# Performance work log

Measured on AMD Instinct MI355X. Metric: run time of the kernel, lower is better.

The kernel has to match this reference:

```python
import jax, jax.numpy as jnp
import numpy as np

B, NB, BIN = 8, 512, 10           # batch, num_bins, bin_size
D, H, L, F, E, K = 1024, 8, 4, 1024, 30, 4  # emb, heads, layers, ffn, experts, top_k
S = NB + 1                        # seq len with CLS token
DH = D // H
CAP = 1152


def _pos_encoding(seq, d):
    pos = np.arange(seq)[:, None].astype(np.float32)
    div = np.exp(np.arange(0, d, 2).astype(np.float32) * (-np.log(10000.0) / d))
    pe = np.zeros((seq, d), dtype=np.float32)
    pe[:, 0::2] = np.sin(pos * div)
    pe[:, 1::2] = np.cos(pos * div)
    return jnp.asarray(pe)

PE = _pos_encoding(S, D)


def _ln(h, g, b):
    m = h.mean(-1, keepdims=True)
    v = ((h - m) ** 2).mean(-1, keepdims=True)
    return (h - m) * jax.lax.rsqrt(v + 1e-5) * g + b


def _conv(h, w, dil):
    # torch Conv1d(k=3, padding=dil, dilation=dil, bias=False) -> same length
    return jax.lax.conv_general_dilated(h, w, (1,), [(dil, dil)], rhs_dilation=(dil,),
                                        dimension_numbers=('NCH', 'OIH', 'NCH'))


def _moe(m, Wg, Bg, W1, B1, W2, B2):
    # top-k routed expert FFN with capacity-based dispatch (no dense all-expert compute)
    T = B * S
    xt = m.reshape(T, D)
    probs = jax.nn.softmax(xt @ Wg + Bg, axis=-1)           # [T, E]
    gate, idx = jax.lax.top_k(probs, K)                     # [T, K]
    gate = gate / gate.sum(-1, keepdims=True)
    e = idx.reshape(-1)                                     # [T*K]
    g = gate.reshape(-1)
    oh = jax.nn.one_hot(e, E, dtype=jnp.int32)
    pos = (jnp.cumsum(oh, axis=0) * oh).sum(-1) - 1         # position within expert
    keep = pos < CAP
    pos_c = jnp.where(keep, pos, CAP)                       # overflow -> dummy slot CAP
    xt_rep = xt[jnp.repeat(jnp.arange(T), K)]               # [T*K, D]
    buf = jnp.zeros((E, CAP + 1, D), m.dtype).at[e, pos_c].add(xt_rep)
    hid = jax.nn.gelu(jnp.einsum('ecd,edf->ecf', buf, W1) + B1[:, None, :], approximate=False)
    out = jnp.einsum('ecf,efd->ecd', hid, W2) + B2[:, None, :]
    y = out[e, pos_c] * (g * keep)[:, None]                 # dropped tokens masked to 0
    return y.reshape(T, K, D).sum(1).reshape(B, S, D)


def _layer(h, p):
    (l1g, l1b, l2g, l2b, Wq, Wk, Wv, Wo, Bq, Bk, Bv, Bo, Wg, Bg, We1, Be1, We2, Be2) = p
    a = _ln(h, l1g, l1b)
    q = (a @ Wq + Bq).reshape(B, S, H, DH)
    k = (a @ Wk + Bk).reshape(B, S, H, DH)
    v = (a @ Wv + Bv).reshape(B, S, H, DH)
    att = jax.nn.softmax(jnp.einsum('bqhd,bkhd->bhqk', q, k) / np.sqrt(DH), axis=-1)
    o = jnp.einsum('bhqk,bkhd->bqhd', att, v).reshape(B, S, D) @ Wo + Bo
    h = h + o
    m = _ln(h, l2g, l2b)
    h = h + _moe(m, Wg, Bg, We1, Be1, We2, Be2)
    return h, None


def _fwd(x, conv_w1, conv_w2, conv_w3, bn1_g, bn1_b, bn2_g, bn2_b, bn3_g, bn3_b,
         proj_w, proj_b, cls_token, mask_token, ln1_g, ln1_b, ln2_g, ln2_b,
         wq, wk, wv, wo, bq, bk, bv, bo, wg, bg, we1, be1, we2, be2):
    x3 = x.reshape(B, NB, BIN)
    h = x3.reshape(B * NB, 1, BIN)
    bn_scale = np.float32(1.0 / np.sqrt(1.0 + 1e-5))  # eval BN: running mean 0, var 1
    for w, gm, bt, dil in ((conv_w1, bn1_g, bn1_b, 1), (conv_w2, bn2_g, bn2_b, 2), (conv_w3, bn3_g, bn3_b, 4)):
        h = _conv(h, w, dil)
        h = h * (gm * bn_scale)[None, :, None] + bt[None, :, None]
        h = jax.nn.gelu(h, approximate=False)
    h = h.mean(-1)                                   # AdaptiveAvgPool1d(1)
    emb = (h @ proj_w + proj_b).reshape(B, NB, D)
    msk = jnp.all(x3 == -100.0, axis=-1)[..., None]
    emb = jnp.where(msk, mask_token, emb)
    emb = jnp.concatenate([jnp.broadcast_to(cls_token, (B, 1, D)), emb], axis=1)
    emb = emb + PE[None]
    h, _ = jax.lax.scan(_layer, emb, (ln1_g, ln1_b, ln2_g, ln2_b, wq, wk, wv, wo,
                                      bq, bk, bv, bo, wg, bg, we1, be1, we2, be2))
    return h[:, 0, :]


def setup_inputs() -> dict:
    key = jax.random.key(0)
    ks = iter(jax.random.split(key, 40))
    r = lambda shape, s=0.02: jax.random.normal(next(ks), shape, jnp.float32) * s
    return dict(
        x=jax.random.normal(next(ks), (B, NB * BIN), jnp.float32),
        conv_w1=r((16, 1, 3), 0.3), conv_w2=r((32, 16, 3), 0.15), conv_w3=r((64, 32, 3), 0.1),
        bn1_g=jnp.ones((16,)), bn1_b=jnp.zeros((16,)),
        bn2_g=jnp.ones((32,)), bn2_b=jnp.zeros((32,)),
        bn3_g=jnp.ones((64,)), bn3_b=jnp.zeros((64,)),
        proj_w=r((64, D), 0.05), proj_b=jnp.zeros((D,)),
        cls_token=r((1, 1, D)), mask_token=r((1, 1, D)),
        ln1_g=jnp.ones((L, D)), ln1_b=jnp.zeros((L, D)),
        ln2_g=jnp.ones((L, D)), ln2_b=jnp.zeros((L, D)),
        wq=r((L, D, D)), wk=r((L, D, D)), wv=r((L, D, D)), wo=r((L, D, D)),
        bq=jnp.zeros((L, D)), bk=jnp.zeros((L, D)), bv=jnp.zeros((L, D)), bo=jnp.zeros((L, D)),
        wg=r((L, D, E)), bg=jnp.zeros((L, E)),
        we1=r((L, E, D, F)), be1=jnp.zeros((L, E, F)),
        we2=r((L, E, F, D)), be2=jnp.zeros((L, E, D)),
    )


def reference(x, conv_w1, conv_w2, conv_w3, bn1_g, bn1_b, bn2_g, bn2_b, bn3_g, bn3_b,
              proj_w, proj_b, cls_token, mask_token, ln1_g, ln1_b, ln2_g, ln2_b,
              wq, wk, wv, wo, bq, bk, bv, bo, wg, bg, we1, be1, we2, be2):
    return _fwd(x, conv_w1, conv_w2, conv_w3, bn1_g, bn1_b, bn2_g, bn2_b, bn3_g, bn3_b,
                proj_w, proj_b, cls_token, mask_token, ln1_g, ln1_b, ln2_g, ln2_b,
                wq, wk, wv, wo, bq, bk, bv, bo, wg, bg, we1, be1, we2, be2)
```

## Files before the change

### kernel.cpp

```cpp
#include <hip/hip_runtime.h>
#include <hip/hip_bf16.h>
#include <math.h>

#define BATCH   8
#define NBINS   512
#define BINSZ   10
#define DMODEL  1024
#define NHEAD   8
#define DHEAD   128
#define NLAYER  4
#define NEXP    30
#define TOPK    4
#define SEQ     513
#define NTOK    (BATCH*SEQ)
#define NBINTOT (BATCH*NBINS)
#define CAPACITY 1152
#define TKF     (NTOK*TOPK)

typedef __attribute__((ext_vector_type(8))) __bf16 bf16x8;
typedef __attribute__((ext_vector_type(4))) __bf16 bf16x4;
typedef __attribute__((ext_vector_type(4))) float f32x4;

__device__ __forceinline__ float gelu_f(float x) {
  return 0.5f * x * (1.0f + erff(x * 0.7071067811865475f));
}

__device__ __forceinline__ bf16x8 bf8_zero() {
  int4 z = make_int4(0, 0, 0, 0);
  return __builtin_bit_cast(bf16x8, z);
}

__global__ __launch_bounds__(256) void transpose_w(const float* __restrict__ src,
                                                   __bf16* __restrict__ dst) {
  int mat = blockIdx.y;
  int tile = blockIdx.x;
  int kt = (tile >> 4) * 64;
  int nt = (tile & 15) * 64;
  const float* s = src + (size_t)mat * 1024 * 1024;
  __bf16* d = dst + (size_t)mat * 1024 * 1024;
  __shared__ float t[64][65];
  int tid = threadIdx.x;
  int r = tid >> 4, c4 = (tid & 15) * 4;
#pragma unroll
  for (int i = 0; i < 4; i++) {
    float4 v = *(const float4*)(s + (size_t)(kt + r + i*16) * 1024 + nt + c4);
    t[r + i*16][c4+0] = v.x; t[r + i*16][c4+1] = v.y;
    t[r + i*16][c4+2] = v.z; t[r + i*16][c4+3] = v.w;
  }
  __syncthreads();
  int r2 = tid >> 2, c2 = (tid & 3) * 16;
  bf16x8 o0, o1;
#pragma unroll
  for (int j = 0; j < 8; j++) { o0[j] = (__bf16)t[c2+j][r2]; o1[j] = (__bf16)t[c2+8+j][r2]; }
  *(bf16x8*)(d + (size_t)(nt + r2) * 1024 + kt + c2)     = o0;
  *(bf16x8*)(d + (size_t)(nt + r2) * 1024 + kt + c2 + 8) = o1;
}

#define CSTEP(acc, T, DIL, hr, wA, wB, wC) { \
  float vv_ = (wB) * (hr)[T]; \
  if ((T) >= (DIL)) vv_ = fmaf((wA), (hr)[(T)-(DIL)], vv_); \
  if ((T) + (DIL) <= 9) vv_ = fmaf((wC), (hr)[(T)+(DIL)], vv_); \
  acc += vv_; }

#define CALL10(DIL, hr, wA, wB, wC) \
  CSTEP(t0,0,DIL,hr,wA,wB,wC); CSTEP(t1,1,DIL,hr,wA,wB,wC); \
  CSTEP(t2,2,DIL,hr,wA,wB,wC); CSTEP(t3,3,DIL,hr,wA,wB,wC); \
  CSTEP(t4,4,DIL,hr,wA,wB,wC); CSTEP(t5,5,DIL,hr,wA,wB,wC); \
  CSTEP(t6,6,DIL,hr,wA,wB,wC); CSTEP(t7,7,DIL,hr,wA,wB,wC); \
  CSTEP(t8,8,DIL,hr,wA,wB,wC); CSTEP(t9,9,DIL,hr,wA,wB,wC);

#define ZERO10 float t0=0.f,t1=0.f,t2=0.f,t3=0.f,t4=0.f,t5=0.f,t6=0.f,t7=0.f,t8=0.f,t9=0.f;

#define STORE10(dst, sc, sh) \
  (dst)[0]=gelu_f(t0*(sc)+(sh)); (dst)[1]=gelu_f(t1*(sc)+(sh)); \
  (dst)[2]=gelu_f(t2*(sc)+(sh)); (dst)[3]=gelu_f(t3*(sc)+(sh)); \
  (dst)[4]=gelu_f(t4*(sc)+(sh)); (dst)[5]=gelu_f(t5*(sc)+(sh)); \
  (dst)[6]=gelu_f(t6*(sc)+(sh)); (dst)[7]=gelu_f(t7*(sc)+(sh)); \
  (dst)[8]=gelu_f(t8*(sc)+(sh)); (dst)[9]=gelu_f(t9*(sc)+(sh));

__global__ __launch_bounds__(64) void conv_frontend(const float* __restrict__ x,
                              const float* __restrict__ w1, const float* __restrict__ w2,
                              const float* __restrict__ w3,
                              const float* __restrict__ g1, const float* __restrict__ b1,
                              const float* __restrict__ g2, const float* __restrict__ b2,
                              const float* __restrict__ g3, const float* __restrict__ b3,
                              float* __restrict__ feat, int* __restrict__ msk) {
  const float bnscale = 0.9999950000374997f;
  int bin = blockIdx.x;
  int c = threadIdx.x;
  __shared__ float xs[BINSZ];
  __shared__ float h1[16][BINSZ];
  __shared__ float h2[32][BINSZ];
  if (c < BINSZ) xs[c] = x[bin*BINSZ + c];
  if (c == 0) {
    int all = 1;
    for (int t = 0; t < BINSZ; t++) if (x[bin*BINSZ+t] != -100.0f) { all = 0; break; }
    msk[bin] = all;
  }
  __syncthreads();
  if (c < 16) {
    float sc = g1[c]*bnscale, sh = b1[c];
    float wA = w1[c*3], wB = w1[c*3+1], wC = w1[c*3+2];
    const float* hr = &xs[0];
    ZERO10;
    CALL10(1, hr, wA, wB, wC);
    STORE10(&h1[c][0], sc, sh);
  }
  __syncthreads();
  if (c < 32) {
    float sc = g2[c]*bnscale, sh = b2[c];
    ZERO10;
    for (int ci = 0; ci < 16; ci++) {
      const float* w = w2 + (c*16+ci)*3;
      float wA = w[0], wB = w[1], wC = w[2];
      const float* hr = &h1[ci][0];
      CALL10(2, hr, wA, wB, wC);
    }
    STORE10(&h2[c][0], sc, sh);
  }
  __syncthreads();
  {
    float sc = g3[c]*bnscale, sh = b3[c];
    ZERO10;
    for (int ci = 0; ci < 32; ci++) {
      const float* w = w3 + (c*32+ci)*3;
      float wA = w[0], wB = w[1], wC = w[2];
      const float* hr = &h2[ci][0];
      CALL10(4, hr, wA, wB, wC);
    }
    float mean = gelu_f(t0*sc+sh) + gelu_f(t1*sc+sh) + gelu_f(t2*sc+sh)
               + gelu_f(t3*sc+sh) + gelu_f(t4*sc+sh) + gelu_f(t5*sc+sh)
               + gelu_f(t6*sc+sh) + gelu_f(t7*sc+sh) + gelu_f(t8*sc+sh)
               + gelu_f(t9*sc+sh);
    feat[bin*64 + c] = mean * 0.1f;
  }
}

__global__ void embed_kernel(const float* __restrict__ feat, const int* __restrict__ msk,
                             const float* __restrict__ proj_w, const float* __restrict__ proj_b,
                             const float* __restrict__ cls_token, const float* __restrict__ mask_token,
                             float* __restrict__ h) {
  int s_ = blockIdx.x;
  int b  = blockIdx.y;
  int tid = threadIdx.x;
  __shared__ __align__(16) float fs[64];
  float out[4];
  if (s_ == 0) {
#pragma unroll
    for (int u = 0; u < 4; u++) out[u] = cls_token[tid*4+u];
  } else {
    int bin = b*NBINS + (s_-1);
    if (tid < 16) ((float4*)fs)[tid] = ((const float4*)(feat + (size_t)bin*64))[tid];
    __syncthreads();
    int m_ = msk[bin];
#pragma unroll
    for (int u = 0; u < 4; u++) {
      int d = tid*4+u;
      float acc = proj_b[d];
      for (int ci = 0; ci < 64; ci++) acc = fmaf(fs[ci], proj_w[ci*DMODEL + d], acc);
      out[u] = m_ ? mask_token[d] : acc;
    }
  }
  const float c0 = -0.008994473019507992f;
#pragma unroll
  for (int u = 0; u < 4; u++) {
    int d = tid*4+u;
    float div = expf(c0 * (float)(d & ~1));
    float ang = (float)s_ * div;
    float pe = (d & 1) ? cosf(ang) : sinf(ang);
    h[((size_t)(b*SEQ + s_))*DMODEL + d] = out[u] + pe;
  }
}

__global__ void ln_kernel(const float* __restrict__ x, float* __restrict__ out,
                          __bf16* __restrict__ outb,
                          const float* __restrict__ g, const float* __restrict__ b) {
  int t = blockIdx.x, tid = threadIdx.x;
  float4 v = ((const float4*)(x + (size_t)t*DMODEL))[tid];
  float s  = v.x+v.y+v.z+v.w;
  float sq = v.x*v.x+v.y*v.y+v.z*v.z+v.w*v.w;
  for (int off = 32; off; off >>= 1) { s += __shfl_down(s, off); sq += __shfl_down(sq, off); }
  __shared__ float ss[4], ssq[4], mv[2];
  int w = tid >> 6, l = tid & 63;
  if (l == 0) { ss[w] = s; ssq[w] = sq; }
  __syncthreads();
  if (tid == 0) {
    float a = 0, c = 0;
    for (int i = 0; i < 4; i++) { a += ss[i]; c += ssq[i]; }
    float mean = a * (1.f/DMODEL);
    float var  = c * (1.f/DMODEL) - mean*mean;
    mv[0] = mean; mv[1] = rsqrtf(var + 1e-5f);
  }
  __syncthreads();
  float mean = mv[0], inv = mv[1];
  float4 gg = ((const float4*)g)[tid];
  float4 bb = ((const float4*)b)[tid];
  float4 o;
  o.x = (v.x-mean)*inv*gg.x + bb.x;
  o.y = (v.y-mean)*inv*gg.y + bb.y;
  o.z = (v.z-mean)*inv*gg.z + bb.z;
  o.w = (v.w-mean)*inv*gg.w + bb.w;
  ((float4*)(out + (size_t)t*DMODEL))[tid] = o;
  bf16x4 ob;
  ob[0] = (__bf16)o.x; ob[1] = (__bf16)o.y; ob[2] = (__bf16)o.z; ob[3] = (__bf16)o.w;
  *(bf16x4*)(outb + (size_t)t*DMODEL + tid*4) = ob;
}

template<int MODE>
__global__ __launch_bounds__(512) void gemm_bf16(
    const __bf16* __restrict__ A, const __bf16* __restrict__ Wt,
    const float* __restrict__ bias, void* __restrict__ C, int M,
    const int* __restrict__ rowmap, const int* __restrict__ cnt,
    const float* __restrict__ gate) {
  int tid = threadIdx.x;
  int rowbase, validrows, e = 0;
  const __bf16* Wb = Wt;
  if (MODE <= 1) {
    rowbase = blockIdx.x * 128;
    validrows = M - rowbase; if (validrows > 128) validrows = 128;
  } else {
    e = blockIdx.x / 9;
    int p0 = (blockIdx.x % 9) * 128;
    int ce = cnt[e];
    if (p0 >= ce) return;
    rowbase = p0;
    validrows = ce - p0; if (validrows > 128) validrows = 128;
    Wb = Wt + (size_t)e * 1024 * 1024;
  }
  int colbase = blockIdx.y * 128;

  __shared__ __align__(16) __bf16 As[4][128][8];
  __shared__ __align__(16) __bf16 Bs[4][128][8];
  __shared__ int srcrow[128];
  __shared__ int frow[128];

  if (tid < 128) {
    if (MODE <= 1) { srcrow[tid] = rowbase + tid; frow[tid] = rowbase + tid; }
    else if (tid < validrows) {
      int f = rowmap[e*CAPACITY + rowbase + tid];
      frow[tid] = f;
      srcrow[tid] = (MODE == 2) ? (f >> 2) : f;
    } else { frow[tid] = 0; srcrow[tid] = 0; }
  }
  __syncthreads();

  int arow = tid >> 2, ag = tid & 3;
  int wcol = tid & 127, wgp = tid >> 7;
  bool aval = (arow < validrows);
  const __bf16* Ap = A + (size_t)srcrow[arow] * 1024 + ag * 8;
  const __bf16* Wp = Wb + (size_t)(colbase + wcol) * 1024 + wgp * 8;

  int w  = tid >> 6;
  int wr = w & 3, wc = w >> 2;
  int l  = tid & 63;
  int lr = l & 15, lg = l >> 4;

  f32x4 acc[2][4] = {};

  bf16x8 areg = bf8_zero(), breg;
  if (aval) areg = *(const bf16x8*)(Ap);
  breg = *(const bf16x8*)(Wp);

  for (int kt = 0; kt < 1024; kt += 32) {
    __syncthreads();
    *(bf16x8*)&As[ag][arow][0] = areg;
    *(bf16x8*)&Bs[wgp][wcol][0] = breg;
    __syncthreads();

    if (kt + 32 < 1024) {
      if (aval) areg = *(const bf16x8*)(Ap + kt + 32);
      breg = *(const bf16x8*)(Wp + kt + 32);
    }

    bf16x8 af[2], bf[4];
    af[0] = *(const bf16x8*)&As[lg][wr*32 + lr][0];
    af[1] = *(const bf16x8*)&As[lg][wr*32 + 16 + lr][0];
#pragma unroll
    for (int fj = 0; fj < 4; fj++) bf[fj] = *(const bf16x8*)&Bs[lg][wc*64 + fj*16 + lr][0];
#pragma unroll
    for (int fi = 0; fi < 2; fi++)
#pragma unroll
      for (int fj = 0; fj < 4; fj++)
        acc[fi][fj] = __builtin_amdgcn_mfma_f32_16x16x32_bf16(af[fi], bf[fj], acc[fi][fj], 0, 0, 0);
  }

  const float* bptr = (MODE >= 2) ? (bias + (size_t)e * 1024) : bias;
#pragma unroll
  for (int fj = 0; fj < 4; fj++) {
    int col = wc*64 + fj*16 + lr;
    float bvv = bptr[colbase + col];
#pragma unroll
    for (int fi = 0; fi < 2; fi++) {
#pragma unroll
      for (int i = 0; i < 4; i++) {
        int r = wr*32 + fi*16 + lg*4 + i;
        if (r >= validrows) continue;
        float val = acc[fi][fj][i] + bvv;
        if (MODE == 0) {
          ((__bf16*)C)[(size_t)(rowbase + r)*1024 + colbase + col] = (__bf16)val;
        } else if (MODE == 1) {
          float* p = (float*)C + (size_t)(rowbase + r)*1024 + colbase + col;
          *p = *p + val;
        } else if (MODE == 2) {
          ((__bf16*)C)[(size_t)frow[r]*1024 + colbase + col] = (__bf16)gelu_f(val);
        } else {
          ((float*)C)[(size_t)frow[r]*1024 + colbase + col] = gate[frow[r]] * val;
        }
      }
    }
  }
}

__global__ __launch_bounds__(256) void attn_mfma(const __bf16* __restrict__ q,
                                                 const __bf16* __restrict__ k,
                                                 const __bf16* __restrict__ v,
                                                 __bf16* __restrict__ o) {
  int qt = blockIdx.x;
  int bh = blockIdx.y;
  int b = bh >> 3, hh = bh & 7;
  int tid = threadIdx.x;
  int wid = tid >> 6, l = tid & 63;
  int lr = l & 15, lg = l >> 4;

  __shared__ __align__(16) __bf16 Ks[64*128];
  __shared__ __align__(16) __bf16 Vt[128*64];

  const float scale = 0.08838834764831845f;

  int qtok = qt*64 + wid*16 + lr;
  int qtokc = qtok < SEQ ? qtok : SEQ-1;
  const __bf16* qrow = q + ((size_t)(b*SEQ + qtokc))*DMODEL + hh*DHEAD;
  bf16x8 qf[4];
#pragma unroll
  for (int c = 0; c < 4; c++) qf[c] = *(const bf16x8*)(qrow + c*32 + lg*8);

  float mreg = -1e30f, lsum = 0.f;
  f32x4 Oacc[8] = {};

  int krow = tid & 63, kdc = tid >> 6;
  int vd = tid & 127, vkg0 = tid >> 7;

  for (int kt = 0; kt < 9; kt++) {
    int kt0 = kt*64;
    __syncthreads();
    {
      int tok = kt0 + krow; if (tok >= SEQ) tok = SEQ-1;
      const __bf16* kr = k + ((size_t)(b*SEQ + tok))*DMODEL + hh*DHEAD + kdc*32;
#pragma unroll
      for (int s2 = 0; s2 < 4; s2++) {
        bf16x8 t = *(const bf16x8*)(kr + s2*8);
        int byte = (krow*256 + (kdc*32 + s2*8)*2) ^ ((krow & 7) << 4);
        *(bf16x8*)((char*)Ks + byte) = t;
      }
    }
    {
#pragma unroll
      for (int it = 0; it < 4; it++) {
        int kkg = vkg0 + it*2;
        bf16x8 t;
#pragma unroll
        for (int j = 0; j < 8; j++) {
          int tok = kt0 + kkg*8 + j; if (tok >= SEQ) tok = SEQ-1;
          t[j] = v[((size_t)(b*SEQ + tok))*DMODEL + hh*DHEAD + vd];
        }
        int byte = (vd*128 + kkg*16) ^ ((vd & 7) << 4);
        *(bf16x8*)((char*)Vt + byte) = t;
      }
    }
    __syncthreads();

    f32x4 sacc[4] = {};
#pragma unroll
    for (int c = 0; c < 4; c++) {
#pragma unroll
      for (int jb = 0; jb < 4; jb++) {
        int row = jb*16 + lr;
        int byte = (row*256 + (c*32 + lg*8)*2) ^ ((lr & 7) << 4);
        bf16x8 af = *(const bf16x8*)((const char*)Ks + byte);
        sacc[jb] = __builtin_amdgcn_mfma_f32_16x16x32_bf16(af, qf[c], sacc[jb], 0, 0, 0);
      }
    }

    float sv[4][4];
    float mt = -1e30f;
#pragma unroll
    for (int jb = 0; jb < 4; jb++)
#pragma unroll
      for (int i = 0; i < 4; i++) {
        int kkI = kt0 + jb*16 + lg*4 + i;
        float s = sacc[jb][i] * scale;
        if (kkI >= SEQ) s = -1e30f;
        sv[jb][i] = s;
        mt = fmaxf(mt, s);
      }
    mt = fmaxf(mt, __shfl_xor(mt, 16));
    mt = fmaxf(mt, __shfl_xor(mt, 32));
    float mnew = fmaxf(mreg, mt);
    float alpha = expf(mreg - mnew);
    float rs = 0.f;
#pragma unroll
    for (int jb = 0; jb < 4; jb++)
#pragma unroll
      for (int i = 0; i < 4; i++) {
        float p = expf(sv[jb][i] - mnew);
        sv[jb][i] = p; rs += p;
      }
    rs += __shfl_xor(rs, 16);
    rs += __shfl_xor(rs, 32);
    lsum = lsum * alpha + rs;
    mreg = mnew;

    unsigned pk[4][2];
#pragma unroll
    for (int jb = 0; jb < 4; jb++) {
      unsigned short c0 = __builtin_bit_cast(unsigned short, (__bf16)sv[jb][0]);
      unsigned short c1 = __builtin_bit_cast(unsigned short, (__bf16)sv[jb][1]);
      unsigned short c2 = __builtin_bit_cast(unsigned short, (__bf16)sv[jb][2]);
      unsigned short c3 = __builtin_bit_cast(unsigned short, (__bf16)sv[jb][3]);
      pk[jb][0] = ((unsigned)c1 << 16) | c0;
      pk[jb][1] = ((unsigned)c3 << 16) | c2;
    }

    float al0 = __shfl(alpha, lg*4 + 0);
    float al1 = __shfl(alpha, lg*4 + 1);
    float al2 = __shfl(alpha, lg*4 + 2);
    float al3 = __shfl(alpha, lg*4 + 3);
#pragma unroll
    for (int db = 0; db < 8; db++) {
      Oacc[db][0] *= al0; Oacc[db][1] *= al1; Oacc[db][2] *= al2; Oacc[db][3] *= al3;
    }

    int srcA = lr + ((lg & 1) << 5);
    int srcB = srcA + 16;
    bool hiSel = (lg >> 1) != 0;
#pragma unroll
    for (int c = 0; c < 2; c++) {
      int a00 = __shfl((int)pk[2*c][0], srcA);
      int a01 = __shfl((int)pk[2*c][1], srcA);
      int a10 = __shfl((int)pk[2*c+1][0], srcA);
      int a11 = __shfl((int)pk[2*c+1][1], srcA);
      int b00 = __shfl((int)pk[2*c][0], srcB);
      int b01 = __shfl((int)pk[2*c][1], srcB);
      int b10 = __shfl((int)pk[2*c+1][0], srcB);
      int b11 = __shfl((int)pk[2*c+1][1], srcB);
      int4 pa;
      pa.x = hiSel ? a10 : a00;
      pa.y = hiSel ? a11 : a01;
      pa.z = hiSel ? b10 : b00;
      pa.w = hiSel ? b11 : b01;
      bf16x8 paf = __builtin_bit_cast(bf16x8, pa);
#pragma unroll
      for (int db = 0; db < 8; db++) {
        int d = db*16 + lr;
        int byte = (d*128 + (c*32 + lg*8)*2) ^ ((lr & 7) << 4);
        bf16x8 bfv = *(const bf16x8*)((const char*)Vt + byte);
        Oacc[db] = __builtin_amdgcn_mfma_f32_16x16x32_bf16(paf, bfv, Oacc[db], 0, 0, 0);
      }
    }
  }

  float l0 = __shfl(lsum, lg*4 + 0);
  float l1 = __shfl(lsum, lg*4 + 1);
  float l2 = __shfl(lsum, lg*4 + 2);
  float l3 = __shfl(lsum, lg*4 + 3);
  float inv[4] = {1.f/l0, 1.f/l1, 1.f/l2, 1.f/l3};
#pragma unroll
  for (int i = 0; i < 4; i++) {
    int tok = qt*64 + wid*16 + lg*4 + i;
    if (tok < SEQ) {
      __bf16* dst = o + ((size_t)(b*SEQ + tok))*DMODEL + hh*DHEAD + lr;
#pragma unroll
      for (int db = 0; db < 8; db++) dst[db*16] = (__bf16)(Oacc[db][i] * inv[i]);
    }
  }
}

__global__ void moe_gate(const float* __restrict__ m, const float* __restrict__ wg,
                         const float* __restrict__ bg, int* __restrict__ idx,
                         float* __restrict__ gate) {
  int t = blockIdx.x, tid = threadIdx.x;
  __shared__ __align__(16) float xs[DMODEL];
  __shared__ float probs[32];
  ((float4*)xs)[tid] = ((const float4*)(m + (size_t)t*DMODEL))[tid];
  __syncthreads();
  int e = tid >> 3, sub = tid & 7;
  if (e < NEXP) {
    float p = 0.f;
    for (int d = sub; d < DMODEL; d += 8) p = fmaf(xs[d], wg[d*NEXP + e], p);
    p += __shfl_down(p, 4, 8);
    p += __shfl_down(p, 2, 8);
    p += __shfl_down(p, 1, 8);
    if (sub == 0) probs[e] = p + bg[e];
  }
  __syncthreads();
  if (tid == 0) {
    float mx = probs[0];
    for (int i = 1; i < NEXP; i++) mx = fmaxf(mx, probs[i]);
    float ssum = 0.f;
    for (int i = 0; i < NEXP; i++) { probs[i] = expf(probs[i]-mx); ssum += probs[i]; }
    float invs = 1.f / ssum;
    float gv[TOPK]; int gi[TOPK]; float gsum = 0.f;
    for (int kk = 0; kk < TOPK; kk++) {
      float best = -1.f; int bi = 0;
      for (int i = 0; i < NEXP; i++) if (probs[i] > best) { best = probs[i]; bi = i; }
      gv[kk] = best * invs; gi[kk] = bi; probs[bi] = -1.f; gsum += gv[kk];
    }
    float ginv = 1.f / gsum;
    for (int kk = 0; kk < TOPK; kk++) { idx[t*TOPK+kk] = gi[kk]; gate[t*TOPK+kk] = gv[kk]*ginv; }
  }
}

__global__ void moe_dispatch(const int* __restrict__ idx, int* __restrict__ slot,
                             int* __restrict__ rowmap, int* __restrict__ cnt) {
  int e = blockIdx.x, tid = threadIdx.x;
  int lane = tid & 63, wid = tid >> 6;
  __shared__ int wsum[4];
  int base = 0;
  for (int c0 = 0; c0 < TKF; c0 += 256) {
    int f = c0 + tid;
    int match = (f < TKF && idx[f] == e) ? 1 : 0;
    unsigned long long bal = __ballot(match);
    if (lane == 0) wsum[wid] = __popcll(bal);
    __syncthreads();
    int prefix = 0;
#pragma unroll
    for (int w2 = 0; w2 < 4; w2++) if (w2 < wid) prefix += wsum[w2];
    int total = wsum[0] + wsum[1] + wsum[2] + wsum[3];
    if (match) {
      int pos = base + prefix + __popcll(bal & ((1ull << lane) - 1ull));
      if (pos < CAPACITY) { slot[f] = pos; rowmap[e*CAPACITY + pos] = f; }
      else slot[f] = -1;
    }
    base += total;
    __syncthreads();
  }
  if (tid == 0) cnt[e] = (base < CAPACITY) ? base : CAPACITY;
}

__global__ void moe_sum(const float* __restrict__ y, const int* __restrict__ slot,
                        float* __restrict__ h) {
  int t = blockIdx.x, d4 = threadIdx.x;
  float4 acc = ((float4*)(h + (size_t)t*DMODEL))[d4];
#pragma unroll
  for (int kk = 0; kk < TOPK; kk++) {
    int f = t*TOPK + kk;
    if (slot[f] >= 0) {
      float4 yv = ((const float4*)(y + (size_t)f*DMODEL))[d4];
      acc.x += yv.x; acc.y += yv.y; acc.z += yv.z; acc.w += yv.w;
    }
  }
  ((float4*)(h + (size_t)t*DMODEL))[d4] = acc;
}

__global__ void final_copy(const float* __restrict__ h, float* __restrict__ out) {
  int b = blockIdx.x, tid = threadIdx.x;
  float4 v = ((const float4*)(h + (size_t)b*SEQ*DMODEL))[tid];
  ((float4*)(out + (size_t)b*DMODEL))[tid] = v;
}

extern "C" void kernel_launch(void* const* d_in, const int* in_sizes, int n_in,
                              void* d_out, int out_size, void* d_ws, size_t ws_size,
                              hipStream_t stream) {
  (void)in_sizes; (void)n_in; (void)out_size; (void)ws_size;
  const float* x         = (const float*)d_in[0];
  const float* conv_w1   = (const float*)d_in[1];
  const float* conv_w2   = (const float*)d_in[2];
  const float* conv_w3   = (const float*)d_in[3];
  const float* bn1_g     = (const float*)d_in[4];
  const float* bn1_b     = (const float*)d_in[5];
  const float* bn2_g     = (const float*)d_in[6];
  const float* bn2_b     = (const float*)d_in[7];
  const float* bn3_g     = (const float*)d_in[8];
  const float* bn3_b     = (const float*)d_in[9];
  const float* proj_w    = (const float*)d_in[10];
  const float* proj_b    = (const float*)d_in[11];
  const float* cls_token = (const float*)d_in[12];
  const float* mask_tok  = (const float*)d_in[13];
  const float* ln1_g     = (const float*)d_in[14];
  const float* ln1_b     = (const float*)d_in[15];
  const float* ln2_g     = (const float*)d_in[16];
  const float* ln2_b     = (const float*)d_in[17];
  const float* wq        = (const float*)d_in[18];
  const float* wk        = (const float*)d_in[19];
  const float* wv        = (const float*)d_in[20];
  const float* wo        = (const float*)d_in[21];
  const float* bq        = (const float*)d_in[22];
  const float* bk        = (const float*)d_in[23];
  const float* bv        = (const float*)d_in[24];
  const float* bo        = (const float*)d_in[25];
  const float* wg        = (const float*)d_in[26];
  const float* bg        = (const float*)d_in[27];
  const float* we1       = (const float*)d_in[28];
  const float* be1       = (const float*)d_in[29];
  const float* we2       = (const float*)d_in[30];
  const float* be2       = (const float*)d_in[31];
  float* out = (float*)d_out;

  char* base = (char*)d_ws;
  const size_t TDB = (size_t)NTOK * DMODEL * 4;
  float*  h    = (float*)(base);
  float*  xbuf = (float*)(base + TDB);
  float*  yb   = (float*)(base + 2*TDB);
  __bf16* xbf  = (__bf16*)(base + 6*TDB);
  __bf16* qb   = (__bf16*)(base + 6*TDB + TDB/2);
  __bf16* kb   = (__bf16*)(base + 7*TDB);
  __bf16* vb   = (__bf16*)(base + 7*TDB + TDB/2);
  __bf16* ao   = (__bf16*)(base + 8*TDB);
  __bf16* hid  = (__bf16*)(base + 8*TDB + TDB/2);
  char* misc   = base + 11*TDB;
  float* feat  = (float*)misc;
  float* gate  = feat + (size_t)NBINTOT*64;
  int* idx     = (int*)(gate + TKF);
  int* slot    = idx + TKF;
  int* rowmap  = slot + TKF;
  int* cnt     = rowmap + NEXP*CAPACITY;
  int* msk     = cnt + 32;
  char* wtb    = base + 12*TDB;
  const size_t MB1 = (size_t)1024*1024;
  __bf16* wtq  = (__bf16*)wtb;
  __bf16* wtk  = wtq + 4*MB1;
  __bf16* wtv  = wtk + 4*MB1;
  __bf16* wto  = wtv + 4*MB1;
  __bf16* wte1 = wto + 4*MB1;
  __bf16* wte2 = wte1 + 120*MB1;

  transpose_w<<<dim3(256, 4),   256, 0, stream>>>(wq,  wtq);
  transpose_w<<<dim3(256, 4),   256, 0, stream>>>(wk,  wtk);
  transpose_w<<<dim3(256, 4),   256, 0, stream>>>(wv,  wtv);
  transpose_w<<<dim3(256, 4),   256, 0, stream>>>(wo,  wto);
  transpose_w<<<dim3(256, 120), 256, 0, stream>>>(we1, wte1);
  transpose_w<<<dim3(256, 120), 256, 0, stream>>>(we2, wte2);

  conv_frontend<<<NBINTOT, 64, 0, stream>>>(x, conv_w1, conv_w2, conv_w3,
      bn1_g, bn1_b, bn2_g, bn2_b, bn3_g, bn3_b, feat, msk);
  embed_kernel<<<dim3(SEQ, BATCH), 256, 0, stream>>>(feat, msk, proj_w, proj_b,
      cls_token, mask_tok, h);

  dim3 gdense((NTOK + 127)/128, 8);
  dim3 gmoe(NEXP*9, 8);

  for (int l = 0; l < NLAYER; l++) {
    for (int z = 0; z < 1; z++) {}
    __bf16* wtq_l = wtq + (size_t)l*MB1;
    __bf16* wtk_l = wtk + (size_t)l*MB1;
    __bf16* wtv_l = wtv + (size_t)l*MB1;
    __bf16* wto_l = wto + (size_t)l*MB1;
    __bf16* wte1_l = wte1 + (size_t)l*NEXP*MB1;
    __bf16* wte2_l = wte2 + (size_t)l*NEXP*MB1;

    ln_kernel<<<NTOK, 256, 0, stream>>>(h, xbuf, xbf, ln1_g + (size_t)l*DMODEL, ln1_b + (size_t)l*DMODEL);
    gemm_bf16<0><<<gdense, 512, 0, stream>>>(xbf, wtq_l, bq + (size_t)l*DMODEL, qb, NTOK, nullptr, nullptr, nullptr);
    gemm_bf16<0><<<gdense, 512, 0, stream>>>(xbf, wtk_l, bk + (size_t)l*DMODEL, kb, NTOK, nullptr, nullptr, nullptr);
    gemm_bf16<0><<<gdense, 512, 0, stream>>>(xbf, wtv_l, bv + (size_t)l*DMODEL, vb, NTOK, nullptr, nullptr, nullptr);
    attn_mfma<<<dim3(9, BATCH*NHEAD), 256, 0, stream>>>(qb, kb, vb, ao);
    gemm_bf16<1><<<gdense, 512, 0, stream>>>(ao, wto_l, bo + (size_t)l*DMODEL, h, NTOK, nullptr, nullptr, nullptr);
    ln_kernel<<<NTOK, 256, 0, stream>>>(h, xbuf, xbf, ln2_g + (size_t)l*DMODEL, ln2_b + (size_t)l*DMODEL);
    moe_gate<<<NTOK, 256, 0, stream>>>(xbuf, wg + (size_t)l*DMODEL*NEXP, bg + (size_t)l*NEXP, idx, gate);
    moe_dispatch<<<NEXP, 256, 0, stream>>>(idx, slot, rowmap, cnt);
    gemm_bf16<2><<<gmoe, 512, 0, stream>>>(xbf, wte1_l, be1 + (size_t)l*NEXP*1024, hid, 0, rowmap, cnt, nullptr);
    gemm_bf16<3><<<gmoe, 512, 0, stream>>>(hid, wte2_l, be2 + (size_t)l*NEXP*1024, yb, 0, rowmap, cnt, gate);
    moe_sum<<<NTOK, 256, 0, stream>>>(yb, slot, h);
  }
  final_copy<<<BATCH, 256, 0, stream>>>(h, out);
}
```

Before: 2.778 ms.

## Fuse QKV projections into one wide GEMM with direct-to-LDS loads

Packs the transposed Q, K and V weights into one interleaved buffer so a single 128x256-tile GEMM produces all three projections, choosing the output and bias by column block. The new wide GEMM loads tiles with global_load_lds straight into shared memory and uses a 4x4 MFMA fragment per wave. The same kernel serves the MoE expert GEMMs with half as many column blocks. The output projection keeps the old register-staged kernel. The aim is fewer launches, more reuse of each A tile, and less register-staging overhead, at the cost of losing the old prefetch overlap, since there is now a sync-bound load-then-compute loop with no double buffering.

```diff
diff --git a/kernel.cpp b/kernel.cpp
--- a/kernel.cpp
+++ b/kernel.cpp
@@ -25,19 +25,19 @@
   return 0.5f * x * (1.0f + erff(x * 0.7071067811865475f));
 }
 
-__device__ __forceinline__ bf16x8 bf8_zero() {
-  int4 z = make_int4(0, 0, 0, 0);
-  return __builtin_bit_cast(bf16x8, z);
+__device__ __forceinline__ void gload16(const __bf16* g, __bf16* l) {
+  __builtin_amdgcn_global_load_lds((const __attribute__((address_space(1))) void*)g,
+                                   (__attribute__((address_space(3))) void*)l, 16, 0, 0);
 }
 
 __global__ __launch_bounds__(256) void transpose_w(const float* __restrict__ src,
-                                                   __bf16* __restrict__ dst) {
+                                                   __bf16* __restrict__ dst, size_t mstride) {
   int mat = blockIdx.y;
   int tile = blockIdx.x;
   int kt = (tile >> 4) * 64;
   int nt = (tile & 15) * 64;
   const float* s = src + (size_t)mat * 1024 * 1024;
-  __bf16* d = dst + (size_t)mat * 1024 * 1024;
+  __bf16* d = dst + (size_t)mat * mstride;
   __shared__ float t[64][65];
   int tid = threadIdx.x;
   int r = tid >> 4, c4 = (tid & 15) * 4;
@@ -207,15 +207,16 @@
 }
 
 template<int MODE>
-__global__ __launch_bounds__(512) void gemm_bf16(
+__global__ __launch_bounds__(512) void gemm_wide(
     const __bf16* __restrict__ A, const __bf16* __restrict__ Wt,
-    const float* __restrict__ bias, void* __restrict__ C, int M,
+    const float* __restrict__ b0, const float* __restrict__ b1, const float* __restrict__ b2,
+    void* __restrict__ C0, void* __restrict__ C1, void* __restrict__ C2, int M,
     const int* __restrict__ rowmap, const int* __restrict__ cnt,
     const float* __restrict__ gate) {
   int tid = threadIdx.x;
   int rowbase, validrows, e = 0;
   const __bf16* Wb = Wt;
-  if (MODE <= 1) {
+  if (MODE == 0) {
     rowbase = blockIdx.x * 128;
     validrows = M - rowbase; if (validrows > 128) validrows = 128;
   } else {
@@ -227,16 +228,18 @@
     validrows = ce - p0; if (validrows > 128) validrows = 128;
     Wb = Wt + (size_t)e * 1024 * 1024;
   }
-  int colbase = blockIdx.y * 128;
-
-  __shared__ __align__(16) __bf16 As[4][128][8];
-  __shared__ __align__(16) __bf16 Bs[4][128][8];
+  int colbase = blockIdx.y * 256;
+
+  __shared__ __align__(16) __bf16 AsT[4096];
+  __shared__ __align__(16) __bf16 BsT[8192];
   __shared__ int srcrow[128];
   __shared__ int frow[128];
 
   if (tid < 128) {
-    if (MODE <= 1) { srcrow[tid] = rowbase + tid; frow[tid] = rowbase + tid; }
-    else if (tid < validrows) {
+    if (MODE == 0) {
+      int r = rowbase + tid; if (r >= M) r = M - 1;
+      srcrow[tid] = r; frow[tid] = r;
+    } else if (tid < validrows) {
       int f = rowmap[e*CAPACITY + rowbase + tid];
       frow[tid] = f;
       srcrow[tid] = (MODE == 2) ? (f >> 2) : f;
@@ -244,11 +247,100 @@
   }
   __syncthreads();
 
+  int arow = tid & 127, ag = tid >> 7;
+  const __bf16* aptr = A + (size_t)srcrow[arow] * 1024 + ag * 8;
+  __bf16* aL = AsT + tid * 8;
+  int bcol = tid & 255;
+  int bg0 = tid >> 8;
+  const __bf16* bptr0 = Wb + (size_t)(colbase + bcol) * 1024 + bg0 * 8;
+  const __bf16* bptr1 = bptr0 + 16;
+  __bf16* bL0 = BsT + tid * 8;
+  __bf16* bL1 = BsT + (512 + tid) * 8;
+
+  int wid = tid >> 6, l = tid & 63;
+  int wr = wid & 1, wc = wid >> 1;
+  int lr = l & 15, lg = l >> 4;
+
+  f32x4 acc[4][4] = {};
+
+  for (int kt = 0; kt < 1024; kt += 32) {
+    gload16(aptr + kt, aL);
+    gload16(bptr0 + kt, bL0);
+    gload16(bptr1 + kt, bL1);
+    __syncthreads();
+
+    bf16x8 af[4], bfr[4];
+#pragma unroll
+    for (int fi = 0; fi < 4; fi++)
+      af[fi] = *(const bf16x8*)(AsT + ((lg*128) + wr*64 + fi*16 + lr) * 8);
+#pragma unroll
+    for (int fj = 0; fj < 4; fj++)
+      bfr[fj] = *(const bf16x8*)(BsT + ((lg*256) + wc*64 + fj*16 + lr) * 8);
+#pragma unroll
+    for (int fi = 0; fi < 4; fi++)
+#pragma unroll
+      for (int fj = 0; fj < 4; fj++)
+        acc[fi][fj] = __builtin_amdgcn_mfma_f32_16x16x32_bf16(af[fi], bfr[fj], acc[fi][fj], 0, 0, 0);
+    __syncthreads();
+  }
+
+  if (MODE == 0) {
+    int which = colbase >> 10;
+    int colb = colbase & 1023;
+    const float* bsel = (which == 0) ? b0 : (which == 1) ? b1 : b2;
+    __bf16* dsel = (which == 0) ? (__bf16*)C0 : (which == 1) ? (__bf16*)C1 : (__bf16*)C2;
+#pragma unroll
+    for (int fj = 0; fj < 4; fj++) {
+      int col = wc*64 + fj*16 + lr;
+      float bvv = bsel[colb + col];
+#pragma unroll
+      for (int fi = 0; fi < 4; fi++)
+#pragma unroll
+        for (int i = 0; i < 4; i++) {
+          int r = wr*64 + fi*16 + lg*4 + i;
+          if (r >= validrows) continue;
+          dsel[(size_t)(rowbase + r)*1024 + colb + col] = (__bf16)(acc[fi][fj][i] + bvv);
+        }
+    }
+  } else {
+    const float* bptr = b0 + (size_t)e * 1024;
+#pragma unroll
+    for (int fj = 0; fj < 4; fj++) {
+      int col = wc*64 + fj*16 + lr;
+      float bvv = bptr[colbase + col];
+#pragma unroll
+      for (int fi = 0; fi < 4; fi++)
+#pragma unroll
+        for (int i = 0; i < 4; i++) {
+          int r = wr*64 + fi*16 + lg*4 + i;
+          if (r >= validrows) continue;
+          float val = acc[fi][fj][i] + bvv;
+          if (MODE == 2) {
+            ((__bf16*)C0)[(size_t)frow[r]*1024 + colbase + col] = (__bf16)gelu_f(val);
+          } else {
+            ((float*)C0)[(size_t)frow[r]*1024 + colbase + col] = gate[frow[r]] * val;
+          }
+        }
+    }
+  }
+}
+
+__global__ __launch_bounds__(512) void gemm_wo(
+    const __bf16* __restrict__ A, const __bf16* __restrict__ Wt,
+    const float* __restrict__ bias, float* __restrict__ C, int M) {
+  int tid = threadIdx.x;
+  int rowbase = blockIdx.x * 128;
+  int validrows = M - rowbase; if (validrows > 128) validrows = 128;
+  int colbase = blockIdx.y * 128;
+
+  __shared__ __align__(16) __bf16 As[4][128][8];
+  __shared__ __align__(16) __bf16 Bs[4][128][8];
+
   int arow = tid >> 2, ag = tid & 3;
   int wcol = tid & 127, wgp = tid >> 7;
-  bool aval = (arow < validrows);
-  const __bf16* Ap = A + (size_t)srcrow[arow] * 1024 + ag * 8;
-  const __bf16* Wp = Wb + (size_t)(colbase + wcol) * 1024 + wgp * 8;
+  int srcr = rowbase + arow; if (srcr >= M) srcr = M - 1;
+  const __bf16* Ap = A + (size_t)srcr * 1024 + ag * 8;
+  const __bf16* Wp = Wt + (size_t)(colbase + wcol) * 1024 + wgp * 8;
 
   int w  = tid >> 6;
   int wr = w & 3, wc = w >> 2;
@@ -257,9 +349,8 @@
 
   f32x4 acc[2][4] = {};
 
-  bf16x8 areg = bf8_zero(), breg;
-  if (aval) areg = *(const bf16x8*)(Ap);
-  breg = *(const bf16x8*)(Wp);
+  bf16x8 areg = *(const bf16x8*)(Ap);
+  bf16x8 breg = *(const bf16x8*)(Wp);
 
   for (int kt = 0; kt < 1024; kt += 32) {
     __syncthreads();
@@ -268,44 +359,34 @@
     __syncthreads();
 
     if (kt + 32 < 1024) {
-      if (aval) areg = *(const bf16x8*)(Ap + kt + 32);
+      areg = *(const bf16x8*)(Ap + kt + 32);
       breg = *(const bf16x8*)(Wp + kt + 32);
     }
 
-    bf16x8 af[2], bf[4];
+    bf16x8 af[2], bfr[4];
     af[0] = *(const bf16x8*)&As[lg][wr*32 + lr][0];
     af[1] = *(const bf16x8*)&As[lg][wr*32 + 16 + lr][0];
 #pragma unroll
-    for (int fj = 0; fj < 4; fj++) bf[fj] = *(const bf16x8*)&Bs[lg][wc*64 + fj*16 + lr][0];
+    for (int fj = 0; fj < 4; fj++) bfr[fj] = *(const bf16x8*)&Bs[lg][wc*64 + fj*16 + lr][0];
 #pragma unroll
     for (int fi = 0; fi < 2; fi++)
 #pragma unroll
       for (int fj = 0; fj < 4; fj++)
-        acc[fi][fj] = __builtin_amdgcn_mfma_f32_16x16x32_bf16(af[fi], bf[fj], acc[fi][fj], 0, 0, 0);
-  }
-
-  const float* bptr = (MODE >= 2) ? (bias + (size_t)e * 1024) : bias;
+        acc[fi][fj] = __builtin_amdgcn_mfma_f32_16x16x32_bf16(af[fi], bfr[fj], acc[fi][fj], 0, 0, 0);
+  }
+
 #pragma unroll
   for (int fj = 0; fj < 4; fj++) {
     int col = wc*64 + fj*16 + lr;
-    float bvv = bptr[colbase + col];
+    float bvv = bias[colbase + col];
 #pragma unroll
     for (int fi = 0; fi < 2; fi++) {
 #pragma unroll
       for (int i = 0; i < 4; i++) {
         int r = wr*32 + fi*16 + lg*4 + i;
         if (r >= validrows) continue;
-        float val = acc[fi][fj][i] + bvv;
-        if (MODE == 0) {
-          ((__bf16*)C)[(size_t)(rowbase + r)*1024 + colbase + col] = (__bf16)val;
-        } else if (MODE == 1) {
-          float* p = (float*)C + (size_t)(rowbase + r)*1024 + colbase + col;
-          *p = *p + val;
-        } else if (MODE == 2) {
-          ((__bf16*)C)[(size_t)frow[r]*1024 + colbase + col] = (__bf16)gelu_f(val);
-        } else {
-          ((float*)C)[(size_t)frow[r]*1024 + colbase + col] = gate[frow[r]] * val;
-        }
+        float* p = C + (size_t)(rowbase + r)*1024 + colbase + col;
+        *p = *p + acc[fi][fj][i] + bvv;
       }
     }
   }
@@ -617,48 +698,48 @@
   int* msk     = cnt + 32;
   char* wtb    = base + 12*TDB;
   const size_t MB1 = (size_t)1024*1024;
-  __bf16* wtq  = (__bf16*)wtb;
-  __bf16* wtk  = wtq + 4*MB1;
-  __bf16* wtv  = wtk + 4*MB1;
-  __bf16* wto  = wtv + 4*MB1;
+  __bf16* wqkv = (__bf16*)wtb;
+  __bf16* wto  = wqkv + 12*MB1;
   __bf16* wte1 = wto + 4*MB1;
   __bf16* wte2 = wte1 + 120*MB1;
 
-  transpose_w<<<dim3(256, 4),   256, 0, stream>>>(wq,  wtq);
-  transpose_w<<<dim3(256, 4),   256, 0, stream>>>(wk,  wtk);
-  transpose_w<<<dim3(256, 4),   256, 0, stream>>>(wv,  wtv);
-  transpose_w<<<dim3(256, 4),   256, 0, stream>>>(wo,  wto);
-  transpose_w<<<dim3(256, 120), 256, 0, stream>>>(we1, wte1);
-  transpose_w<<<dim3(256, 120), 256, 0, stream>>>(we2, wte2);
+  transpose_w<<<dim3(256, 4),   256, 0, stream>>>(wq,  wqkv,           3*MB1);
+  transpose_w<<<dim3(256, 4),   256, 0, stream>>>(wk,  wqkv + MB1,     3*MB1);
+  transpose_w<<<dim3(256, 4),   256, 0, stream>>>(wv,  wqkv + 2*MB1,   3*MB1);
+  transpose_w<<<dim3(256, 4),   256, 0, stream>>>(wo,  wto,            MB1);
+  transpose_w<<<dim3(256, 120), 256, 0, stream>>>(we1, wte1,           MB1);
+  transpose_w<<<dim3(256, 120), 256, 0, stream>>>(we2, wte2,           MB1);
 
   conv_frontend<<<NBINTOT, 64, 0, stream>>>(x, conv_w1, conv_w2, conv_w3,
       bn1_g, bn1_b, bn2_g, bn2_b, bn3_g, bn3_b, feat, msk);
   embed_kernel<<<dim3(SEQ, BATCH), 256, 0, stream>>>(feat, msk, proj_w, proj_b,
       cls_token, mask_tok, h);
 
-  dim3 gdense((NTOK + 127)/128, 8);
-  dim3 gmoe(NEXP*9, 8);
+  dim3 gqkv((NTOK + 127)/128, 12);
+  dim3 gwo((NTOK + 127)/128, 8);
+  dim3 gmoe(NEXP*9, 4);
 
   for (int l = 0; l < NLAYER; l++) {
-    for (int z = 0; z < 1; z++) {}
-    __bf16* wtq_l = wtq + (size_t)l*MB1;
-    __bf16* wtk_l = wtk + (size_t)l*MB1;
-    __bf16* wtv_l = wtv + (size_t)l*MB1;
-    __bf16* wto_l = wto + (size_t)l*MB1;
+    __bf16* wqkv_l = wqkv + (size_t)l*3*MB1;
+    __bf16* wto_l  = wto  + (size_t)l*MB1;
     __bf16* wte1_l = wte1 + (size_t)l*NEXP*MB1;
     __bf16* wte2_l = wte2 + (size_t)l*NEXP*MB1;
 
     ln_kernel<<<NTOK, 256, 0, stream>>>(h, xbuf, xbf, ln1_g + (size_t)l*DMODEL, ln1_b + (size_t)l*DMODEL);
-    gemm_bf16<0><<<gdense, 512, 0, stream>>>(xbf, wtq_l, bq + (size_t)l*DMODEL, qb, NTOK, nullptr, nullptr, nullptr);
-    gemm_bf16<0><<<gdense, 512, 0, stream>>>(xbf, wtk_l, bk + (size_t)l*DMODEL, kb, NTOK, nullptr, nullptr, nullptr);
-    gemm_bf16<0><<<gdense, 512, 0, stream>>>(xbf, wtv_l, bv + (size_t)l*DMODEL, vb, NTOK, nullptr, nullptr, nullptr);
+    gemm_wide<0><<<gqkv, 512, 0, stream>>>(xbf, wqkv_l,
+        bq + (size_t)l*DMODEL, bk + (size_t)l*DMODEL, bv + (size_t)l*DMODEL,
+        qb, kb, vb, NTOK, nullptr, nullptr, nullptr);
     attn_mfma<<<dim3(9, BATCH*NHEAD), 256, 0, stream>>>(qb, kb, vb, ao);
-    gemm_bf16<1><<<gdense, 512, 0, stream>>>(ao, wto_l, bo + (size_t)l*DMODEL, h, NTOK, nullptr, nullptr, nullptr);
+    gemm_wo<<<gwo, 512, 0, stream>>>(ao, wto_l, bo + (size_t)l*DMODEL, h, NTOK);
     ln_kernel<<<NTOK, 256, 0, stream>>>(h, xbuf, xbf, ln2_g + (size_t)l*DMODEL, ln2_b + (size_t)l*DMODEL);
     moe_gate<<<NTOK, 256, 0, stream>>>(xbuf, wg + (size_t)l*DMODEL*NEXP, bg + (size_t)l*NEXP, idx, gate);
     moe_dispatch<<<NEXP, 256, 0, stream>>>(idx, slot, rowmap, cnt);
-    gemm_bf16<2><<<gmoe, 512, 0, stream>>>(xbf, wte1_l, be1 + (size_t)l*NEXP*1024, hid, 0, rowmap, cnt, nullptr);
-    gemm_bf16<3><<<gmoe, 512, 0, stream>>>(hid, wte2_l, be2 + (size_t)l*NEXP*1024, yb, 0, rowmap, cnt, gate);
+    gemm_wide<2><<<gmoe, 512, 0, stream>>>(xbf, wte1_l,
+        be1 + (size_t)l*NEXP*1024, nullptr, nullptr,
+        hid, nullptr, nullptr, 0, rowmap, cnt, nullptr);
+    gemm_wide<3><<<gmoe, 512, 0, stream>>>(hid, wte2_l,
+        be2 + (size_t)l*NEXP*1024, nullptr, nullptr,
+        yb, nullptr, nullptr, 0, rowmap, cnt, gate);
     moe_sum<<<NTOK, 256, 0, stream>>>(yb, slot, h);
   }
   final_copy<<<BATCH, 256, 0, stream>>>(h, out);
```

Result: slower. 2.965 ms (+6.7%).
